# Performance work log

Hardware: AMD Instinct MI355X
Metric: run time of the kernel (lower is better)

The kernel has to match this reference:

```python
import jax, jax.numpy as jnp
import numpy as np

B, T, P, D, H = 4, 12, 196, 512, 8
DH = D // H
EPS = 1e-6


def _norm(x, alpha, bias):
    # torch Norm: alpha*(x-mean)/(std_unbiased+eps)+bias, std uses Bessel correction (ddof=1)
    mu = jnp.mean(x, axis=-1, keepdims=True)
    sd = jnp.std(x, axis=-1, ddof=1, keepdims=True)
    return alpha * (x - mu) / (sd + EPS) + bias


def setup_inputs() -> dict:
    key = jax.random.key(0)
    ks = jax.random.split(key, 12)
    s = 0.02

    def n(k, shape, scale=s):
        return jax.random.normal(k, shape, jnp.float32) * scale

    return {
        "x": jax.random.normal(ks[0], (B, T, P, D), jnp.float32),
        "Wq": n(ks[1], (D, D)), "bq": jnp.zeros((D,), jnp.float32),
        "Wk": n(ks[2], (D, D)), "bk": jnp.zeros((D,), jnp.float32),
        "Wv": n(ks[3], (D, D)), "bv": jnp.zeros((D,), jnp.float32),
        "in_a": jnp.ones((D,), jnp.float32), "in_b": jnp.zeros((D,), jnp.float32),
        "attn_a": jnp.ones((D,), jnp.float32), "attn_b": jnp.zeros((D,), jnp.float32),
        "out_a": jnp.ones((D,), jnp.float32), "out_b": jnp.zeros((D,), jnp.float32),
        "Wt": n(ks[4], (T, D, D)), "bt": jnp.zeros((T, D), jnp.float32),
        "pos": n(ks[5], (T, T, P, D), 0.02),
        "W1": n(ks[6], (2 * D, D)), "b1": jnp.zeros((2 * D,), jnp.float32),
        "W2": n(ks[7], (D, 2 * D)), "b2": jnp.zeros((D,), jnp.float32),
    }


def reference(x, Wq, bq, Wk, bk, Wv, bv, in_a, in_b, attn_a, attn_b,
              out_a, out_b, Wt, bt, pos, W1, b1, W2, b2):
    x2 = _norm(x, in_a, in_b)

    def proj(W, b):
        # [B,T,P,D] -> [B,T,H,P,DH]
        return (x2 @ W.T + b).reshape(B, T, P, H, DH).transpose(0, 1, 3, 2, 4)

    Q = proj(Wq, bq)
    K = proj(Wk, bk)
    V = proj(Wv, bv)

    # all-pairs temporal cross attention: [B,t,u,H,Pq,Pk]
    qk = jnp.einsum('btijk,builk->btuijl', Q, K) / np.sqrt(DH)
    attn = jax.nn.softmax(qk, axis=-1)  # no mask, dropout=0
    av = jnp.einsum('btuijl,builk->btuijk', attn, V)  # [B,t,u,H,P,DH]
    av = av.transpose(0, 1, 2, 4, 3, 5).reshape(B, T, T, P, D)
    av = _norm(av, attn_a, attn_b)
    x2p = av + pos  # pos broadcasts over batch

    # per-u Linear fused as one batched contraction, summed over u
    tc = jnp.einsum('btupd,ued->btpe', x2p / T, Wt) + jnp.sum(bt, axis=0)
    x = x + jax.nn.gelu(tc, approximate=False)

    x2 = _norm(x, out_a, out_b)
    h = jax.nn.gelu(x2 @ W1.T + b1, approximate=False)
    y = jax.nn.gelu(h @ W2.T + b2, approximate=False)
    return x + y
```

## Files before the change

kernel.cpp:

```cpp
#include <hip/hip_runtime.h>
#include <hip/hip_bf16.h>

typedef __hip_bfloat16 bf16;

typedef __bf16 bfrag8 __attribute__((ext_vector_type(8)));
typedef __bf16 bfrag4 __attribute__((ext_vector_type(4)));
typedef float  ffrag4 __attribute__((ext_vector_type(4)));
typedef float  ffrag16 __attribute__((ext_vector_type(16)));

#define EPS 1e-6f

__device__ __forceinline__ float gelu_exact(float v) {
  return 0.5f * v * (1.0f + erff(v * 0.7071067811865475f));
}

__device__ __forceinline__ void async16(const void* g, void* s) {
  __builtin_amdgcn_global_load_lds(
      (const __attribute__((address_space(1))) unsigned int*)g,
      (__attribute__((address_space(3))) unsigned int*)s, 16, 0, 0);
}

struct alignas(16) bf16x8 { bf16 v[8]; };
struct alignas(4)  bf16p2 { __bf16 v[2]; };

__global__ __launch_bounds__(256) void zero_acc_kernel(float* __restrict__ p) {
  size_t i = ((size_t)blockIdx.x * 256 + threadIdx.x) * 4;
  *(float4*)(p + i) = make_float4(0.f, 0.f, 0.f, 0.f);
}

__global__ __launch_bounds__(256) void conv_w_kernel(
    const float* __restrict__ Wq, const float* __restrict__ Wk,
    const float* __restrict__ Wv, const float* __restrict__ W1,
    const float* __restrict__ W2, const float* __restrict__ Wt,
    __bf16* __restrict__ dst)
{
  size_t e = ((size_t)blockIdx.x * 256 + threadIdx.x) * 8;
  const float* src; size_t off;
  if      (e <  262144) { src = Wq; off = e; }
  else if (e <  524288) { src = Wk; off = e -  262144; }
  else if (e <  786432) { src = Wv; off = e -  524288; }
  else if (e < 1310720) { src = W1; off = e -  786432; }
  else if (e < 1835008) { src = W2; off = e - 1310720; }
  else if (e < 4980736) { src = Wt; off = e - 1835008; }
  else return;
  float4 f0 = *(const float4*)(src + off);
  float4 f1 = *(const float4*)(src + off + 4);
  bfrag8 o;
  o[0] = (__bf16)f0.x; o[1] = (__bf16)f0.y; o[2] = (__bf16)f0.z; o[3] = (__bf16)f0.w;
  o[4] = (__bf16)f1.x; o[5] = (__bf16)f1.y; o[6] = (__bf16)f1.z; o[7] = (__bf16)f1.w;
  *(bfrag8*)(dst + e) = o;
}

__global__ __launch_bounds__(512) void sum_bt_kernel(
    const float* __restrict__ bt, float* __restrict__ sbt)
{
  int n = threadIdx.x;
  float s = 0.f;
#pragma unroll
  for (int u = 0; u < 12; ++u) s += bt[u * 512 + n];
  sbt[n] = s;
}

__global__ __launch_bounds__(64) void norm_f32_to_bf16_kernel(
    const float* __restrict__ in, __bf16* __restrict__ out,
    const float* __restrict__ alpha, const float* __restrict__ beta)
{
  size_t row = blockIdx.x;
  int l = threadIdx.x;
  const float* r = in + row * 512 + l * 8;
  float4 v0 = *(const float4*)(r);
  float4 v1 = *(const float4*)(r + 4);
  float f[8] = {v0.x, v0.y, v0.z, v0.w, v1.x, v1.y, v1.z, v1.w};
  float s = 0.f, ss = 0.f;
#pragma unroll
  for (int q = 0; q < 8; ++q) { s += f[q]; ss += f[q] * f[q]; }
#pragma unroll
  for (int off = 32; off; off >>= 1) { s += __shfl_xor(s, off); ss += __shfl_xor(ss, off); }
  float mu = s * (1.f / 512.f);
  float var = fmaxf((ss - 512.f * mu * mu) * (1.f / 511.f), 0.f);
  float inv = 1.f / (sqrtf(var) + EPS);
  const float* al = alpha + l * 8;
  const float* be = beta + l * 8;
  float4 a0 = *(const float4*)al, a1 = *(const float4*)(al + 4);
  float4 b0 = *(const float4*)be, b1 = *(const float4*)(be + 4);
  float aa[8] = {a0.x, a0.y, a0.z, a0.w, a1.x, a1.y, a1.z, a1.w};
  float bb[8] = {b0.x, b0.y, b0.z, b0.w, b1.x, b1.y, b1.z, b1.w};
  bfrag8 o;
#pragma unroll
  for (int q = 0; q < 8; ++q) o[q] = (__bf16)(aa[q] * (f[q] - mu) * inv + bb[q]);
  *(bfrag8*)(out + row * 512 + l * 8) = o;
}

__global__ __launch_bounds__(64) void norm_av_kernel(
    bf16* __restrict__ av, const float* __restrict__ alpha,
    const float* __restrict__ beta, const float* __restrict__ pos)
{
  size_t row = blockIdx.x;
  int l = threadIdx.x;
  bf16* r = av + row * 512 + (size_t)l * 8;
  bf16x8 ib = *(const bf16x8*)r;
  float f[8];
#pragma unroll
  for (int q = 0; q < 8; ++q) f[q] = __bfloat162float(ib.v[q]);
  float s = 0.f, ss = 0.f;
#pragma unroll
  for (int q = 0; q < 8; ++q) { s += f[q]; ss += f[q] * f[q]; }
#pragma unroll
  for (int off = 32; off; off >>= 1) { s += __shfl_xor(s, off); ss += __shfl_xor(ss, off); }
  float mu = s * (1.f / 512.f);
  float var = fmaxf((ss - 512.f * mu * mu) * (1.f / 511.f), 0.f);
  float inv = 1.f / (sqrtf(var) + EPS);
  size_t prow = row % 28224;
  const float* pr = pos + prow * 512 + l * 8;
  float4 p0 = *(const float4*)pr, p1 = *(const float4*)(pr + 4);
  const float* al = alpha + l * 8;
  const float* be = beta + l * 8;
  float4 a0 = *(const float4*)al, a1 = *(const float4*)(al + 4);
  float4 b0 = *(const float4*)be, b1 = *(const float4*)(be + 4);
  float pa[8] = {p0.x, p0.y, p0.z, p0.w, p1.x, p1.y, p1.z, p1.w};
  float aa[8] = {a0.x, a0.y, a0.z, a0.w, a1.x, a1.y, a1.z, a1.w};
  float bb[8] = {b0.x, b0.y, b0.z, b0.w, b1.x, b1.y, b1.z, b1.w};
  bf16x8 ob;
#pragma unroll
  for (int q = 0; q < 8; ++q)
    ob.v[q] = __float2bfloat16(aa[q] * (f[q] - mu) * inv + bb[q] + pa[q]);
  *(bf16x8*)r = ob;
}

__global__ __launch_bounds__(256) void mfma_nt_kernel(
    const __bf16* __restrict__ A,
    const __bf16* __restrict__ Bq, const __bf16* __restrict__ Bk,
    const __bf16* __restrict__ Bv,
    const float* __restrict__ bq, const float* __restrict__ bk,
    const float* __restrict__ bv,
    __bf16* __restrict__ oq, __bf16* __restrict__ ok, __bf16* __restrict__ ov,
    const float* __restrict__ res, float* __restrict__ fout,
    int K, int mode)
{
  __shared__ __bf16 As[64 * 32];
  __shared__ __bf16 Bs[128 * 32];
  int tid = threadIdx.x;
  int m0 = blockIdx.y * 64;
  int n0g = blockIdx.x * 128;

  const __bf16* Bsel; const float* biassel; __bf16* osel; int ncol0;
  if (mode == 0) {
    int sel = n0g >> 9;
    Bsel = sel == 0 ? Bq : (sel == 1 ? Bk : Bv);
    biassel = sel == 0 ? bq : (sel == 1 ? bk : bv);
    osel = sel == 0 ? oq : (sel == 1 ? ok : ov);
    ncol0 = n0g & 511;
  } else {
    Bsel = Bq; biassel = bq; osel = oq; ncol0 = n0g;
  }

  int srow = tid >> 2, scol = (tid & 3) * 8;
  const __bf16* a0 = A + (size_t)(m0 + srow) * K + scol;
  const __bf16* b0 = Bsel + (size_t)(ncol0 + srow) * K + scol;
  const __bf16* b1 = Bsel + (size_t)(ncol0 + 64 + srow) * K + scol;
  char* sa0 = (char*)As + tid * 16;
  char* sb0 = (char*)Bs + tid * 16;
  char* sb1 = (char*)Bs + 4096 + tid * 16;

  int l = tid & 63, w = tid >> 6;
  int lm = l & 15, lq = l >> 4;
  int wm = w >> 1, wn = w & 1;

  ffrag4 acc[2][4] = {};
  for (int k0 = 0; k0 < K; k0 += 32) {
    __syncthreads();
    async16(a0 + k0, sa0);
    async16(b0 + k0, sb0);
    async16(b1 + k0, sb1);
    __syncthreads();
    bfrag8 af[2], bfr[4];
#pragma unroll
    for (int i = 0; i < 2; ++i)
      af[i] = *(const bfrag8*)&As[(wm * 32 + i * 16 + lm) * 32 + lq * 8];
#pragma unroll
    for (int j = 0; j < 4; ++j)
      bfr[j] = *(const bfrag8*)&Bs[(wn * 64 + j * 16 + lm) * 32 + lq * 8];
#pragma unroll
    for (int i = 0; i < 2; ++i)
#pragma unroll
      for (int j = 0; j < 4; ++j)
        acc[i][j] = __builtin_amdgcn_mfma_f32_16x16x32_bf16(af[i], bfr[j], acc[i][j], 0, 0, 0);
  }

#pragma unroll
  for (int i = 0; i < 2; ++i) {
    int mbase = m0 + wm * 32 + i * 16 + lq * 4;
#pragma unroll
    for (int j = 0; j < 4; ++j) {
      int n = ncol0 + wn * 64 + j * 16 + lm;
      float bj = biassel[n];
#pragma unroll
      for (int r = 0; r < 4; ++r) {
        int mr = mbase + r;
        float v = acc[i][j][r] + bj;
        if (mode == 0)      osel[(size_t)mr * 512 + n] = (__bf16)v;
        else if (mode == 1) osel[(size_t)mr * 1024 + n] = (__bf16)gelu_exact(v);
        else                fout[(size_t)mr * 512 + n] =
                              res[(size_t)mr * 512 + n] + gelu_exact(v);
      }
    }
  }
}

__global__ __launch_bounds__(256) void mfma_tc_kernel(
    const __bf16* __restrict__ X2p, const __bf16* __restrict__ Wtb,
    float* __restrict__ accb)
{
  __shared__ __bf16 As[64 * 32];
  __shared__ __bf16 Bs[128 * 32];
  int tid = threadIdx.x;
  int m0 = blockIdx.y * 64;
  int n0 = blockIdx.x * 128;
  int ug = blockIdx.z * 3;

  int srow = tid >> 2, scol = (tid & 3) * 8;
  int r0 = m0 + srow;
  int btq0 = r0 / 196, p0 = r0 - btq0 * 196;
  const __bf16* a0 = X2p + (size_t)btq0 * 1204224 + (size_t)p0 * 512 + scol;
  const __bf16* b0 = Wtb + (size_t)(n0 + srow) * 512 + scol;
  const __bf16* b1 = Wtb + (size_t)(n0 + 64 + srow) * 512 + scol;
  char* sa0 = (char*)As + tid * 16;
  char* sb0 = (char*)Bs + tid * 16;
  char* sb1 = (char*)Bs + 4096 + tid * 16;

  int l = tid & 63, w = tid >> 6;
  int lm = l & 15, lq = l >> 4;
  int wm = w >> 1, wn = w & 1;

  ffrag4 acc[2][4] = {};
  for (int u = ug; u < ug + 3; ++u) {
    size_t au = (size_t)u * 100352;
    size_t bu = (size_t)u * 262144;
    for (int d0 = 0; d0 < 512; d0 += 32) {
      __syncthreads();
      async16(a0 + au + d0, sa0);
      async16(b0 + bu + d0, sb0);
      async16(b1 + bu + d0, sb1);
      __syncthreads();
      bfrag8 af[2], bfr[4];
#pragma unroll
      for (int i = 0; i < 2; ++i)
        af[i] = *(const bfrag8*)&As[(wm * 32 + i * 16 + lm) * 32 + lq * 8];
#pragma unroll
      for (int j = 0; j < 4; ++j)
        bfr[j] = *(const bfrag8*)&Bs[(wn * 64 + j * 16 + lm) * 32 + lq * 8];
#pragma unroll
      for (int i = 0; i < 2; ++i)
#pragma unroll
        for (int j = 0; j < 4; ++j)
          acc[i][j] = __builtin_amdgcn_mfma_f32_16x16x32_bf16(af[i], bfr[j], acc[i][j], 0, 0, 0);
    }
  }

#pragma unroll
  for (int i = 0; i < 2; ++i) {
    int mbase = m0 + wm * 32 + i * 16 + lq * 4;
#pragma unroll
    for (int j = 0; j < 4; ++j) {
      int n = n0 + wn * 64 + j * 16 + lm;
#pragma unroll
      for (int r = 0; r < 4; ++r) {
        int mr = mbase + r;
        atomicAdd(accb + (size_t)mr * 512 + n, acc[i][j][r]);
      }
    }
  }
}

__global__ __launch_bounds__(64) void tc_epi_norm_kernel(
    const float* __restrict__ accb, const float* __restrict__ x,
    const float* __restrict__ sbt,
    const float* __restrict__ alpha, const float* __restrict__ beta,
    float* __restrict__ xmid, __bf16* __restrict__ x3b)
{
  size_t row = blockIdx.x;
  int l = threadIdx.x;
  size_t base = row * 512 + l * 8;
  float4 c0 = *(const float4*)(accb + base);
  float4 c1 = *(const float4*)(accb + base + 4);
  float4 x0 = *(const float4*)(x + base);
  float4 x1 = *(const float4*)(x + base + 4);
  float4 s0 = *(const float4*)(sbt + l * 8);
  float4 s1 = *(const float4*)(sbt + l * 8 + 4);
  float cc[8] = {c0.x, c0.y, c0.z, c0.w, c1.x, c1.y, c1.z, c1.w};
  float xx[8] = {x0.x, x0.y, x0.z, x0.w, x1.x, x1.y, x1.z, x1.w};
  float sv[8] = {s0.x, s0.y, s0.z, s0.w, s1.x, s1.y, s1.z, s1.w};
  float f[8];
#pragma unroll
  for (int q = 0; q < 8; ++q)
    f[q] = xx[q] + gelu_exact(cc[q] * (1.f / 12.f) + sv[q]);
  *(float4*)(xmid + base)     = make_float4(f[0], f[1], f[2], f[3]);
  *(float4*)(xmid + base + 4) = make_float4(f[4], f[5], f[6], f[7]);
  float s = 0.f, ss = 0.f;
#pragma unroll
  for (int q = 0; q < 8; ++q) { s += f[q]; ss += f[q] * f[q]; }
#pragma unroll
  for (int off = 32; off; off >>= 1) { s += __shfl_xor(s, off); ss += __shfl_xor(ss, off); }
  float mu = s * (1.f / 512.f);
  float var = fmaxf((ss - 512.f * mu * mu) * (1.f / 511.f), 0.f);
  float inv = 1.f / (sqrtf(var) + EPS);
  const float* al = alpha + l * 8;
  const float* be = beta + l * 8;
  float4 a0 = *(const float4*)al, a1 = *(const float4*)(al + 4);
  float4 b0 = *(const float4*)be, b1 = *(const float4*)(be + 4);
  float aa[8] = {a0.x, a0.y, a0.z, a0.w, a1.x, a1.y, a1.z, a1.w};
  float bb[8] = {b0.x, b0.y, b0.z, b0.w, b1.x, b1.y, b1.z, b1.w};
  bfrag8 o;
#pragma unroll
  for (int q = 0; q < 8; ++q) o[q] = (__bf16)(aa[q] * (f[q] - mu) * inv + bb[q]);
  *(bfrag8*)(x3b + base) = o;
}

__global__ __launch_bounds__(512, 4) void attn_kernel(
    const __bf16* __restrict__ Q, const __bf16* __restrict__ K,
    const __bf16* __restrict__ V, __bf16* __restrict__ av)
{
  __shared__ __bf16 Ks[196 * 64];
  __shared__ __bf16 Vt[64 * 208];
  __shared__ __bf16 Pball[8 * 32 * 20];

  int bid = blockIdx.x;
  int half = bid & 1;
  int h = (bid >> 1) & 7;
  int r0 = bid >> 4;
  int u = r0 % 12;
  int b = r0 / 12;

  const __bf16* Kp = K + ((size_t)(b * 12 + u) * 196) * 512 + h * 64;
  const __bf16* Vp = V + ((size_t)(b * 12 + u) * 196) * 512 + h * 64;

  for (int idx = threadIdx.x; idx < 196 * 8; idx += 512) {
    int r = idx >> 3, g = idx & 7;
    *(bfrag8*)&Ks[r * 64 + ((g ^ (r & 7)) * 8)] =
        *(const bfrag8*)&Kp[(size_t)r * 512 + g * 8];
  }
  for (int idx = threadIdx.x; idx < 64 * 6; idx += 512) {
    int r = idx / 6, c2 = 196 + (idx % 6) * 2;
    bf16p2 z; z.v[0] = (__bf16)0.f; z.v[1] = (__bf16)0.f;
    *(bf16p2*)&Vt[r * 208 + c2] = z;
  }
  for (int idx = threadIdx.x; idx < 98 * 8; idx += 512) {
    int r2 = (idx % 98) * 2, c8 = (idx / 98) * 8;
    bfrag8 va = *(const bfrag8*)&Vp[(size_t)r2 * 512 + c8];
    bfrag8 vb = *(const bfrag8*)&Vp[(size_t)(r2 + 1) * 512 + c8];
#pragma unroll
    for (int e = 0; e < 8; ++e) {
      bf16p2 pr; pr.v[0] = va[e]; pr.v[1] = vb[e];
      *(bf16p2*)&Vt[(c8 + e) * 208 + r2] = pr;
    }
  }
  __syncthreads();

  int w = threadIdx.x >> 6, l = threadIdx.x & 63;
  int l5 = l >> 5, c = l & 31;
  __bf16* Pb = Pball + w * (32 * 20);

  for (int unit = w; unit < 42; unit += 8) {
    int t = unit / 7, qt = unit - t * 7;
    int tq = half * 6 + t;
    const __bf16* Qp = Q + ((size_t)(b * 12 + tq) * 196) * 512 + h * 64;
    __bf16* avp = av + ((size_t)((b * 12 + tq) * 12 + u) * 196) * 512 + h * 64;
    int q0 = qt * 32;

    const __bf16* qp = Qp + (size_t)(q0 + c) * 512 + l5 * 8;
    bfrag8 qf[4];
    qf[0] = *(const bfrag8*)(qp);
    qf[1] = *(const bfrag8*)(qp + 16);
    qf[2] = *(const bfrag8*)(qp + 32);
    qf[3] = *(const bfrag8*)(qp + 48);

    ffrag16 O0, O1;
#pragma unroll
    for (int g = 0; g < 16; ++g) { O0[g] = 0.f; O1[g] = 0.f; }
    float sumacc = 0.f;

    for (int nt = 0; nt < 7; ++nt) {
      int key = nt * 32 + c; if (key > 195) key = 195;
      const __bf16* kbase = &Ks[key * 64];
      int kx = key & 7;

      ffrag16 s;
#pragma unroll
      for (int g = 0; g < 16; ++g) s[g] = 0.f;
#pragma unroll
      for (int kc = 0; kc < 4; ++kc) {
        bfrag8 kf = *(const bfrag8*)&kbase[(((kc * 2 + l5) ^ kx) * 8)];
        s = __builtin_amdgcn_mfma_f32_32x32x16_bf16(kf, qf[kc], s, 0, 0, 0);
      }

#pragma unroll
      for (int g = 0; g < 16; ++g) {
        float e = __expf(s[g] * 0.125f);
        bool keep = (nt < 6) || ((g < 4) && (l5 == 0));
        e = keep ? e : 0.f;
        s[g] = e;
        sumacc += e;
      }

#pragma unroll
      for (int sub = 0; sub < 2; ++sub) {
        if (nt == 6 && sub == 1) break;
#pragma unroll
        for (int g = 0; g < 8; ++g) {
          int gg = sub * 8 + g;
          int k16 = (gg & 3) + 8 * ((gg >> 2) & 1) + 4 * l5;
          Pb[c * 20 + k16] = (__bf16)s[gg];
        }
        __threadfence_block();
        int ch = nt * 2 + sub;
        bfrag4 plo = *(const bfrag4*)&Pb[c * 20 + l5 * 8];
        bfrag4 phi = *(const bfrag4*)&Pb[c * 20 + l5 * 8 + 4];
        bfrag8 pa = __builtin_shufflevector(plo, phi, 0, 1, 2, 3, 4, 5, 6, 7);
        bfrag8 v0 = *(const bfrag8*)&Vt[(size_t)(c     ) * 208 + ch * 16 + l5 * 8];
        bfrag8 v1 = *(const bfrag8*)&Vt[(size_t)(c + 32) * 208 + ch * 16 + l5 * 8];
        O0 = __builtin_amdgcn_mfma_f32_32x32x16_bf16(pa, v0, O0, 0, 0, 0);
        O1 = __builtin_amdgcn_mfma_f32_32x32x16_bf16(pa, v1, O1, 0, 0, 0);
      }
    }

    float stot = sumacc + __shfl_xor(sumacc, 32);

#pragma unroll
    for (int g = 0; g < 16; ++g) {
      int row = (g & 3) + 8 * (g >> 2) + 4 * l5;
      float sq = __shfl(stot, row);
      float iv = __builtin_amdgcn_rcpf(sq);
      int q = q0 + row;
      if (q < 196) {
        size_t base = (size_t)q * 512 + c;
        avp[base]      = (__bf16)(O0[g] * iv);
        avp[base + 32] = (__bf16)(O1[g] * iv);
      }
    }
  }
}

extern "C" void kernel_launch(void* const* d_in, const int* in_sizes, int n_in,
                              void* d_out, int out_size, void* d_ws, size_t ws_size,
                              hipStream_t stream)
{
  const float* x      = (const float*)d_in[0];
  const float* Wq     = (const float*)d_in[1];
  const float* bq     = (const float*)d_in[2];
  const float* Wk     = (const float*)d_in[3];
  const float* bk     = (const float*)d_in[4];
  const float* Wv     = (const float*)d_in[5];
  const float* bv     = (const float*)d_in[6];
  const float* in_a   = (const float*)d_in[7];
  const float* in_b   = (const float*)d_in[8];
  const float* attn_a = (const float*)d_in[9];
  const float* attn_b = (const float*)d_in[10];
  const float* out_a  = (const float*)d_in[11];
  const float* out_b  = (const float*)d_in[12];
  const float* Wt     = (const float*)d_in[13];
  const float* bt     = (const float*)d_in[14];
  const float* pos    = (const float*)d_in[15];
  const float* W1     = (const float*)d_in[16];
  const float* b1     = (const float*)d_in[17];
  const float* W2     = (const float*)d_in[18];
  const float* b2     = (const float*)d_in[19];

  char* ws = (char*)d_ws;
  const size_t bfb = (size_t)9408 * 512 * 2;
  __bf16* x2b  = (__bf16*)(ws);
  __bf16* Qb   = (__bf16*)(ws + bfb);
  __bf16* Kb   = (__bf16*)(ws + 2 * bfb);
  __bf16* Vb   = (__bf16*)(ws + 3 * bfb);
  __bf16* av   = (__bf16*)(ws + 4 * bfb);
  char*   wreg = ws + 4 * bfb + (size_t)115605504;
  __bf16* Wqb  = (__bf16*)(wreg);
  __bf16* Wkb  = (__bf16*)(wreg) + 262144;
  __bf16* Wvb  = (__bf16*)(wreg) + 524288;
  __bf16* W1b  = (__bf16*)(wreg) + 786432;
  __bf16* W2b  = (__bf16*)(wreg) + 1310720;
  __bf16* Wtb  = (__bf16*)(wreg) + 1835008;
  float*  sbt  = (float*)(wreg + 9961472);
  float*  accb = (float*)(wreg + 9963520);
  float*  xmid = (float*)(ws);
  __bf16* x3b  = (__bf16*)(ws + 2 * bfb);
  __bf16* hb   = (__bf16*)(ws + 4 * bfb);
  float*  out  = (float*)d_out;

  conv_w_kernel<<<2432, 256, 0, stream>>>(Wq, Wk, Wv, W1, W2, Wt, (__bf16*)wreg);
  sum_bt_kernel<<<1, 512, 0, stream>>>(bt, sbt);
  zero_acc_kernel<<<4704, 256, 0, stream>>>(accb);
  norm_f32_to_bf16_kernel<<<9408, 64, 0, stream>>>(x, x2b, in_a, in_b);
  mfma_nt_kernel<<<dim3(12, 147), 256, 0, stream>>>(
      x2b, Wqb, Wkb, Wvb, bq, bk, bv, Qb, Kb, Vb, nullptr, nullptr, 512, 0);
  attn_kernel<<<768, 512, 0, stream>>>(Qb, Kb, Vb, av);
  norm_av_kernel<<<112896, 64, 0, stream>>>((bf16*)av, attn_a, attn_b, pos);
  mfma_tc_kernel<<<dim3(4, 147, 4), 256, 0, stream>>>(av, Wtb, accb);
  tc_epi_norm_kernel<<<9408, 64, 0, stream>>>(accb, x, sbt, out_a, out_b, xmid, x3b);
  mfma_nt_kernel<<<dim3(8, 147), 256, 0, stream>>>(
      x3b, W1b, nullptr, nullptr, b1, nullptr, nullptr, hb, nullptr, nullptr,
      nullptr, nullptr, 512, 1);
  mfma_nt_kernel<<<dim3(4, 147), 256, 0, stream>>>(
      hb, W2b, nullptr, nullptr, b2, nullptr, nullptr, nullptr, nullptr, nullptr,
      xmid, out, 1024, 2);
}
```

Baseline: 533.2 us.

## Enlarge GEMM tiles to 128x128, swizzle LDS, relayout Wt, pack norm rows

Doubles the M tile of the MFMA GEMMs to 128 rows, with row clamping and bounds-checked stores, so each B tile is reused across more rows. Adds an XOR swizzle on LDS column chunks to reduce bank conflicts on fragment reads. Relayouts Wt into an [e][u*512+d] layout so the temporal contraction runs as one contiguous K loop per z-split. It also packs four rows per block in the av norm kernel to cut tiny-block launch overhead. The larger tiles raise register pressure, and halving the grid lowers occupancy and the number of blocks available to fill the CUs.

```diff
diff --git a/kernel.cpp b/kernel.cpp
--- a/kernel.cpp
+++ b/kernel.cpp
@@ -35,20 +35,26 @@
     __bf16* __restrict__ dst)
 {
   size_t e = ((size_t)blockIdx.x * 256 + threadIdx.x) * 8;
-  const float* src; size_t off;
-  if      (e <  262144) { src = Wq; off = e; }
-  else if (e <  524288) { src = Wk; off = e -  262144; }
-  else if (e <  786432) { src = Wv; off = e -  524288; }
-  else if (e < 1310720) { src = W1; off = e -  786432; }
-  else if (e < 1835008) { src = W2; off = e - 1310720; }
-  else if (e < 4980736) { src = Wt; off = e - 1835008; }
+  const float* src; size_t off, dsto;
+  if      (e <  262144) { src = Wq; off = e;           dsto = e; }
+  else if (e <  524288) { src = Wk; off = e -  262144; dsto = e; }
+  else if (e <  786432) { src = Wv; off = e -  524288; dsto = e; }
+  else if (e < 1310720) { src = W1; off = e -  786432; dsto = e; }
+  else if (e < 1835008) { src = W2; off = e - 1310720; dsto = e; }
+  else if (e < 4980736) {
+    src = Wt; off = e - 1835008;
+    size_t u = off >> 18;
+    size_t rem = off & 262143;
+    size_t eo = rem >> 9, d = rem & 511;
+    dsto = 1835008 + eo * 6144 + u * 512 + d;
+  }
   else return;
   float4 f0 = *(const float4*)(src + off);
   float4 f1 = *(const float4*)(src + off + 4);
   bfrag8 o;
   o[0] = (__bf16)f0.x; o[1] = (__bf16)f0.y; o[2] = (__bf16)f0.z; o[3] = (__bf16)f0.w;
   o[4] = (__bf16)f1.x; o[5] = (__bf16)f1.y; o[6] = (__bf16)f1.z; o[7] = (__bf16)f1.w;
-  *(bfrag8*)(dst + e) = o;
+  *(bfrag8*)(dst + dsto) = o;
 }
 
 __global__ __launch_bounds__(512) void sum_bt_kernel(
@@ -91,12 +97,12 @@
   *(bfrag8*)(out + row * 512 + l * 8) = o;
 }
 
-__global__ __launch_bounds__(64) void norm_av_kernel(
+__global__ __launch_bounds__(256) void norm_av_kernel(
     bf16* __restrict__ av, const float* __restrict__ alpha,
     const float* __restrict__ beta, const float* __restrict__ pos)
 {
-  size_t row = blockIdx.x;
-  int l = threadIdx.x;
+  size_t row = (size_t)blockIdx.x * 4 + (threadIdx.x >> 6);
+  int l = threadIdx.x & 63;
   bf16* r = av + row * 512 + (size_t)l * 8;
   bf16x8 ib = *(const bf16x8*)r;
   float f[8];
@@ -137,10 +143,10 @@
     const float* __restrict__ res, float* __restrict__ fout,
     int K, int mode)
 {
-  __shared__ __bf16 As[64 * 32];
+  __shared__ __bf16 As[128 * 32];
   __shared__ __bf16 Bs[128 * 32];
   int tid = threadIdx.x;
-  int m0 = blockIdx.y * 64;
+  int m0 = blockIdx.y * 128;
   int n0g = blockIdx.x * 128;
 
   const __bf16* Bsel; const float* biassel; __bf16* osel; int ncol0;
@@ -154,42 +160,49 @@
     Bsel = Bq; biassel = bq; osel = oq; ncol0 = n0g;
   }
 
-  int srow = tid >> 2, scol = (tid & 3) * 8;
-  const __bf16* a0 = A + (size_t)(m0 + srow) * K + scol;
+  int srow = tid >> 2;
+  int scol = ((tid & 3) ^ ((srow >> 1) & 3)) * 8;
+  int rg0 = m0 + srow;       if (rg0 > 9407) rg0 = 9407;
+  int rg1 = m0 + 64 + srow;  if (rg1 > 9407) rg1 = 9407;
+  const __bf16* a0 = A + (size_t)rg0 * K + scol;
+  const __bf16* a1 = A + (size_t)rg1 * K + scol;
   const __bf16* b0 = Bsel + (size_t)(ncol0 + srow) * K + scol;
   const __bf16* b1 = Bsel + (size_t)(ncol0 + 64 + srow) * K + scol;
   char* sa0 = (char*)As + tid * 16;
+  char* sa1 = (char*)As + 4096 + tid * 16;
   char* sb0 = (char*)Bs + tid * 16;
   char* sb1 = (char*)Bs + 4096 + tid * 16;
 
   int l = tid & 63, w = tid >> 6;
   int lm = l & 15, lq = l >> 4;
   int wm = w >> 1, wn = w & 1;
-
-  ffrag4 acc[2][4] = {};
+  int rsw = ((((lm >> 1) & 3) ^ lq)) * 8;
+
+  ffrag4 acc[4][4] = {};
   for (int k0 = 0; k0 < K; k0 += 32) {
     __syncthreads();
     async16(a0 + k0, sa0);
+    async16(a1 + k0, sa1);
     async16(b0 + k0, sb0);
     async16(b1 + k0, sb1);
     __syncthreads();
-    bfrag8 af[2], bfr[4];
-#pragma unroll
-    for (int i = 0; i < 2; ++i)
-      af[i] = *(const bfrag8*)&As[(wm * 32 + i * 16 + lm) * 32 + lq * 8];
+    bfrag8 af[4], bfr[4];
+#pragma unroll
+    for (int i = 0; i < 4; ++i)
+      af[i] = *(const bfrag8*)&As[(wm * 64 + i * 16 + lm) * 32 + rsw];
 #pragma unroll
     for (int j = 0; j < 4; ++j)
-      bfr[j] = *(const bfrag8*)&Bs[(wn * 64 + j * 16 + lm) * 32 + lq * 8];
-#pragma unroll
-    for (int i = 0; i < 2; ++i)
+      bfr[j] = *(const bfrag8*)&Bs[(wn * 64 + j * 16 + lm) * 32 + rsw];
+#pragma unroll
+    for (int i = 0; i < 4; ++i)
 #pragma unroll
       for (int j = 0; j < 4; ++j)
         acc[i][j] = __builtin_amdgcn_mfma_f32_16x16x32_bf16(af[i], bfr[j], acc[i][j], 0, 0, 0);
   }
 
 #pragma unroll
-  for (int i = 0; i < 2; ++i) {
-    int mbase = m0 + wm * 32 + i * 16 + lq * 4;
+  for (int i = 0; i < 4; ++i) {
+    int mbase = m0 + wm * 64 + i * 16 + lq * 4;
 #pragma unroll
     for (int j = 0; j < 4; ++j) {
       int n = ncol0 + wn * 64 + j * 16 + lm;
@@ -197,76 +210,84 @@
 #pragma unroll
       for (int r = 0; r < 4; ++r) {
         int mr = mbase + r;
-        float v = acc[i][j][r] + bj;
-        if (mode == 0)      osel[(size_t)mr * 512 + n] = (__bf16)v;
-        else if (mode == 1) osel[(size_t)mr * 1024 + n] = (__bf16)gelu_exact(v);
-        else                fout[(size_t)mr * 512 + n] =
-                              res[(size_t)mr * 512 + n] + gelu_exact(v);
+        if (mr < 9408) {
+          float v = acc[i][j][r] + bj;
+          if (mode == 0)      osel[(size_t)mr * 512 + n] = (__bf16)v;
+          else if (mode == 1) osel[(size_t)mr * 1024 + n] = (__bf16)gelu_exact(v);
+          else                fout[(size_t)mr * 512 + n] =
+                                res[(size_t)mr * 512 + n] + gelu_exact(v);
+        }
       }
     }
   }
 }
 
 __global__ __launch_bounds__(256) void mfma_tc_kernel(
-    const __bf16* __restrict__ X2p, const __bf16* __restrict__ Wtb,
+    const __bf16* __restrict__ X2p, const __bf16* __restrict__ Wte,
     float* __restrict__ accb)
 {
-  __shared__ __bf16 As[64 * 32];
+  __shared__ __bf16 As[128 * 32];
   __shared__ __bf16 Bs[128 * 32];
   int tid = threadIdx.x;
-  int m0 = blockIdx.y * 64;
+  int m0 = blockIdx.y * 128;
   int n0 = blockIdx.x * 128;
-  int ug = blockIdx.z * 3;
-
-  int srow = tid >> 2, scol = (tid & 3) * 8;
-  int r0 = m0 + srow;
-  int btq0 = r0 / 196, p0 = r0 - btq0 * 196;
-  const __bf16* a0 = X2p + (size_t)btq0 * 1204224 + (size_t)p0 * 512 + scol;
-  const __bf16* b0 = Wtb + (size_t)(n0 + srow) * 512 + scol;
-  const __bf16* b1 = Wtb + (size_t)(n0 + 64 + srow) * 512 + scol;
+  int z  = blockIdx.z;
+
+  int srow = tid >> 2;
+  int scol = ((tid & 3) ^ ((srow >> 1) & 3)) * 8;
+  int rg0 = m0 + srow;       if (rg0 > 9407) rg0 = 9407;
+  int rg1 = m0 + 64 + srow;  if (rg1 > 9407) rg1 = 9407;
+  int btq0 = rg0 / 196, p0_ = rg0 - btq0 * 196;
+  int btq1 = rg1 / 196, p1_ = rg1 - btq1 * 196;
+  const __bf16* a0 = X2p + (size_t)btq0 * 1204224 + (size_t)p0_ * 512 + scol;
+  const __bf16* a1 = X2p + (size_t)btq1 * 1204224 + (size_t)p1_ * 512 + scol;
+  const __bf16* b0 = Wte + (size_t)(n0 + srow) * 6144 + scol;
+  const __bf16* b1 = Wte + (size_t)(n0 + 64 + srow) * 6144 + scol;
   char* sa0 = (char*)As + tid * 16;
+  char* sa1 = (char*)As + 4096 + tid * 16;
   char* sb0 = (char*)Bs + tid * 16;
   char* sb1 = (char*)Bs + 4096 + tid * 16;
 
   int l = tid & 63, w = tid >> 6;
   int lm = l & 15, lq = l >> 4;
   int wm = w >> 1, wn = w & 1;
-
-  ffrag4 acc[2][4] = {};
-  for (int u = ug; u < ug + 3; ++u) {
-    size_t au = (size_t)u * 100352;
-    size_t bu = (size_t)u * 262144;
-    for (int d0 = 0; d0 < 512; d0 += 32) {
-      __syncthreads();
-      async16(a0 + au + d0, sa0);
-      async16(b0 + bu + d0, sb0);
-      async16(b1 + bu + d0, sb1);
-      __syncthreads();
-      bfrag8 af[2], bfr[4];
-#pragma unroll
-      for (int i = 0; i < 2; ++i)
-        af[i] = *(const bfrag8*)&As[(wm * 32 + i * 16 + lm) * 32 + lq * 8];
+  int rsw = ((((lm >> 1) & 3) ^ lq)) * 8;
+
+  ffrag4 acc[4][4] = {};
+  int kbeg = z * 1536, kend = kbeg + 1536;
+  for (int k0 = kbeg; k0 < kend; k0 += 32) {
+    size_t aoff = (size_t)(k0 >> 9) * 100352 + (size_t)(k0 & 511);
+    __syncthreads();
+    async16(a0 + aoff, sa0);
+    async16(a1 + aoff, sa1);
+    async16(b0 + k0, sb0);
+    async16(b1 + k0, sb1);
+    __syncthreads();
+    bfrag8 af[4], bfr[4];
+#pragma unroll
+    for (int i = 0; i < 4; ++i)
+      af[i] = *(const bfrag8*)&As[(wm * 64 + i * 16 + lm) * 32 + rsw];
+#pragma unroll
+    for (int j = 0; j < 4; ++j)
+      bfr[j] = *(const bfrag8*)&Bs[(wn * 64 + j * 16 + lm) * 32 + rsw];
+#pragma unroll
+    for (int i = 0; i < 4; ++i)
 #pragma unroll
       for (int j = 0; j < 4; ++j)
-        bfr[j] = *(const bfrag8*)&Bs[(wn * 64 + j * 16 + lm) * 32 + lq * 8];
-#pragma unroll
-      for (int i = 0; i < 2; ++i)
-#pragma unroll
-        for (int j = 0; j < 4; ++j)
-          acc[i][j] = __builtin_amdgcn_mfma_f32_16x16x32_bf16(af[i], bfr[j], acc[i][j], 0, 0, 0);
-    }
-  }
-
-#pragma unroll
-  for (int i = 0; i < 2; ++i) {
-    int mbase = m0 + wm * 32 + i * 16 + lq * 4;
+        acc[i][j] = __builtin_amdgcn_mfma_f32_16x16x32_bf16(af[i], bfr[j], acc[i][j], 0, 0, 0);
+  }
+
+#pragma unroll
+  for (int i = 0; i < 4; ++i) {
+    int mbase = m0 + wm * 64 + i * 16 + lq * 4;
 #pragma unroll
     for (int j = 0; j < 4; ++j) {
       int n = n0 + wn * 64 + j * 16 + lm;
 #pragma unroll
       for (int r = 0; r < 4; ++r) {
         int mr = mbase + r;
-        atomicAdd(accb + (size_t)mr * 512 + n, acc[i][j][r]);
+        if (mr < 9408)
+          atomicAdd(accb + (size_t)mr * 512 + n, acc[i][j][r]);
       }
     }
   }
@@ -490,16 +511,16 @@
   sum_bt_kernel<<<1, 512, 0, stream>>>(bt, sbt);
   zero_acc_kernel<<<4704, 256, 0, stream>>>(accb);
   norm_f32_to_bf16_kernel<<<9408, 64, 0, stream>>>(x, x2b, in_a, in_b);
-  mfma_nt_kernel<<<dim3(12, 147), 256, 0, stream>>>(
+  mfma_nt_kernel<<<dim3(12, 74), 256, 0, stream>>>(
       x2b, Wqb, Wkb, Wvb, bq, bk, bv, Qb, Kb, Vb, nullptr, nullptr, 512, 0);
   attn_kernel<<<768, 512, 0, stream>>>(Qb, Kb, Vb, av);
-  norm_av_kernel<<<112896, 64, 0, stream>>>((bf16*)av, attn_a, attn_b, pos);
-  mfma_tc_kernel<<<dim3(4, 147, 4), 256, 0, stream>>>(av, Wtb, accb);
+  norm_av_kernel<<<28224, 256, 0, stream>>>((bf16*)av, attn_a, attn_b, pos);
+  mfma_tc_kernel<<<dim3(4, 74, 4), 256, 0, stream>>>(av, Wtb, accb);
   tc_epi_norm_kernel<<<9408, 64, 0, stream>>>(accb, x, sbt, out_a, out_b, xmid, x3b);
-  mfma_nt_kernel<<<dim3(8, 147), 256, 0, stream>>>(
+  mfma_nt_kernel<<<dim3(8, 74), 256, 0, stream>>>(
       x3b, W1b, nullptr, nullptr, b1, nullptr, nullptr, hb, nullptr, nullptr,
       nullptr, nullptr, 512, 1);
-  mfma_nt_kernel<<<dim3(4, 147), 256, 0, stream>>>(
+  mfma_nt_kernel<<<dim3(4, 74), 256, 0, stream>>>(
       hb, W2b, nullptr, nullptr, b2, nullptr, nullptr, nullptr, nullptr, nullptr,
       xmid, out, 1024, 2);
 }
```

New measurement: 571.2 us. +7.1%, slower.
